# Optimization experiments

Measured on AMD Instinct MI355X. Metric: run time of the kernel, lower is better.

Reference implementation:

```python
import jax, jax.numpy as jnp
import numpy as np

HID = 4096
HEADS = 32
HEAD_DIM = 128
SEQ = 2048
GROUP = 128          # AWQ quantization group size along the input (K) dim
QKV_OUT = 3 * HID
ROPE_BASE = 10000.0


def dequant(qweight, scales, zeros):
    # qweight: [K, N] int; scales/zeros: [K//GROUP, N]
    s = jnp.repeat(scales, GROUP, axis=0)
    z = jnp.repeat(zeros, GROUP, axis=0)
    return (qweight.astype(jnp.float32) - z) * s


def rotate_half(x):
    x1, x2 = jnp.split(x, 2, axis=-1)
    return jnp.concatenate((-x2, x1), axis=-1)


def setup_inputs() -> dict:
    key = jax.random.key(0)
    ks = jax.random.split(key, 8)
    hidden_states = jax.random.normal(ks[0], (1, SEQ, HID), dtype=jnp.float32)
    position_ids = jnp.arange(SEQ, dtype=jnp.int32)[None, :]
    qkv_qweight = jax.random.randint(ks[1], (HID, QKV_OUT), 0, 16, dtype=jnp.int32)
    qkv_scales = jax.random.uniform(ks[2], (HID // GROUP, QKV_OUT), dtype=jnp.float32) * 0.002
    qkv_zeros = jax.random.uniform(ks[3], (HID // GROUP, QKV_OUT), dtype=jnp.float32) * 16.0
    o_qweight = jax.random.randint(ks[4], (HID, HID), 0, 16, dtype=jnp.int32)
    o_scales = jax.random.uniform(ks[5], (HID // GROUP, HID), dtype=jnp.float32) * 0.002
    o_zeros = jax.random.uniform(ks[6], (HID // GROUP, HID), dtype=jnp.float32) * 16.0
    return {"hidden_states": hidden_states, "position_ids": position_ids,
            "qkv_qweight": qkv_qweight, "qkv_scales": qkv_scales, "qkv_zeros": qkv_zeros,
            "o_qweight": o_qweight, "o_scales": o_scales, "o_zeros": o_zeros}


def reference(hidden_states, position_ids, qkv_qweight, qkv_scales, qkv_zeros,
              o_qweight, o_scales, o_zeros):
    b, s, _ = hidden_states.shape
    # --- quantized QKV projection (dequant + GEMM) ---
    w_qkv = dequant(qkv_qweight, qkv_scales, qkv_zeros)        # [HID, 3*HID]
    proj = jnp.einsum('bsk,kn->bsn', hidden_states, w_qkv)     # [b, s, 3*HID]
    xqkv = proj.reshape(b, s, 3, HEADS, HEAD_DIM)
    # [b, h, s, d]
    q = jnp.transpose(xqkv[:, :, 0], (0, 2, 1, 3))
    k = jnp.transpose(xqkv[:, :, 1], (0, 2, 1, 3))
    v = jnp.transpose(xqkv[:, :, 2], (0, 2, 1, 3))
    # --- rotary embedding (no KV cache: kv_seq_len == s) ---
    inv_freq = 1.0 / (ROPE_BASE ** (jnp.arange(0, HEAD_DIM, 2, dtype=jnp.float32) / HEAD_DIM))
    t = jnp.arange(s, dtype=jnp.float32)
    freqs = jnp.outer(t, inv_freq)                             # [s, d/2]
    emb = jnp.concatenate((freqs, freqs), axis=-1)             # [s, d]
    cos = jnp.cos(emb)[position_ids][:, None]                  # [b, 1, s, d]
    sin = jnp.sin(emb)[position_ids][:, None]
    q = q * cos + rotate_half(q) * sin
    k = k * cos + rotate_half(k) * sin
    # --- causal attention (flash_attn_func, padding_mask=None branch) ---
    scale = 1.0 / jnp.sqrt(jnp.float32(HEAD_DIM))
    scores = jnp.einsum('bhqd,bhkd->bhqk', q, k) * scale       # [b, h, s, s]
    causal = jnp.tril(jnp.ones((s, s), dtype=bool))
    scores = jnp.where(causal, scores, jnp.float32(-1e30))
    probs = jax.nn.softmax(scores, axis=-1)
    attn = jnp.einsum('bhqk,bhkd->bhqd', probs, v)             # [b, h, s, d]
    attn = jnp.transpose(attn, (0, 2, 1, 3)).reshape(b, s, HID)
    # --- quantized output projection ---
    w_o = dequant(o_qweight, o_scales, o_zeros)                # [HID, HID]
    out = jnp.einsum('bsk,kn->bsn', attn, w_o)                 # [b, s, HID]
    return out
```

## Files before the change

### kernel.cpp

```cpp
#include <hip/hip_runtime.h>
#include <hip/hip_bf16.h>

#define S_LEN 2048
#define HID_DIM 4096
#define NH 32
#define HD 128
#define NQKV 12288

typedef _Float16 half2v __attribute__((ext_vector_type(2)));
typedef _Float16 half4v __attribute__((ext_vector_type(4)));
typedef _Float16 half8v __attribute__((ext_vector_type(8)));
typedef float f32x4 __attribute__((ext_vector_type(4)));

typedef const __attribute__((address_space(1))) unsigned int* gas_u32;
typedef __attribute__((address_space(3))) unsigned int* las_u32;

__device__ inline void g2lds16(const _Float16* g, _Float16* l) {
  __builtin_amdgcn_global_load_lds((gas_u32)g, (las_u32)l, 16, 0, 0);
}

__device__ inline void store_out(_Float16* p, float v) { *p = (_Float16)v; }
__device__ inline void store_out(float* p, float v) { *p = v; }

__global__ __launch_bounds__(256) void dequant_w(const int* __restrict__ W,
                                                 const float* __restrict__ scal,
                                                 const float* __restrict__ zer,
                                                 _Float16* __restrict__ Wt, int K, int N) {
  __shared__ _Float16 lT[64 * 84];
  const int k0 = blockIdx.y * 64, n0 = blockIdx.x * 64;
  const int tid = threadIdx.x, c = tid & 63, rp = tid >> 6;
  const int g = k0 >> 7;
  const float sc = scal[(size_t)g * N + n0 + c];
  const float zp = zer[(size_t)g * N + n0 + c];
#pragma unroll
  for (int i = 0; i < 8; ++i) {
    const int k = i * 8 + rp * 2;
    const float q0 = (float)W[(size_t)(k0 + k) * N + n0 + c];
    const float q1 = (float)W[(size_t)(k0 + k + 1) * N + n0 + c];
    half2v p;
    p[0] = (_Float16)((q0 - zp) * sc);
    p[1] = (_Float16)((q1 - zp) * sc);
    *(half2v*)&lT[c * 84 + k] = p;
  }
  __syncthreads();
  const int kc = tid & 7, nr0 = tid >> 3;
#pragma unroll
  for (int i = 0; i < 2; ++i) {
    const int n = nr0 + 32 * i;
    union { half8v v8; half4v v4[2]; } u;
    u.v4[0] = *(const half4v*)&lT[n * 84 + kc * 8];
    u.v4[1] = *(const half4v*)&lT[n * 84 + kc * 8 + 4];
    *(half8v*)&Wt[(size_t)(n0 + n) * K + k0 + kc * 8] = u.v8;
  }
}

__global__ __launch_bounds__(256) void conv_a(const float* __restrict__ A, _Float16* __restrict__ Af) {
  const int i = blockIdx.x * 256 + threadIdx.x;
  const float4 t = ((const float4*)A)[i];
  half4v r;
  r[0] = (_Float16)t.x; r[1] = (_Float16)t.y; r[2] = (_Float16)t.z; r[3] = (_Float16)t.w;
  ((half4v*)Af)[i] = r;
}

template <typename CT>
__global__ __launch_bounds__(256) void gemm_f16(const _Float16* __restrict__ A,
                                                const _Float16* __restrict__ Bt,
                                                CT* __restrict__ C, int M, int N, int K) {
  __shared__ _Float16 lA[128 * 32];
  __shared__ _Float16 lB[128 * 32];

  const int tid = threadIdx.x;
  const int wave = tid >> 6, lane = tid & 63;
  const int quad = lane >> 4, l16 = lane & 15;
  const int wr = wave >> 1, wc = wave & 1;
  const int mb = blockIdx.y, nb = blockIdx.x;

  f32x4 acc[4][4];
  const f32x4 zero4 = {0.f, 0.f, 0.f, 0.f};
#pragma unroll
  for (int mt = 0; mt < 4; ++mt)
#pragma unroll
    for (int nt = 0; nt < 4; ++nt) acc[mt][nt] = zero4;

  const _Float16* Ab = A + (size_t)(mb * 128) * K;
  const _Float16* Bb = Bt + (size_t)(nb * 128) * K;
  const int lrow = lane >> 2;
  const int lkc = ((lane & 3) ^ ((lane >> 3) & 3)) * 8;
  const int sq = (quad ^ ((l16 >> 1) & 3)) * 8;

  for (int k0 = 0; k0 < K; k0 += 32) {
#pragma unroll
    for (int p = 0; p < 2; ++p) {
      const int issue = wave * 2 + p;
      const int row = issue * 16 + lrow;
      g2lds16(Ab + (size_t)row * K + k0 + lkc, &lA[issue * 512]);
      g2lds16(Bb + (size_t)row * K + k0 + lkc, &lB[issue * 512]);
    }
    __syncthreads();

    half8v af[4], bf[4];
#pragma unroll
    for (int mt = 0; mt < 4; ++mt) af[mt] = *(half8v*)&lA[(wr * 64 + mt * 16 + l16) * 32 + sq];
#pragma unroll
    for (int nt = 0; nt < 4; ++nt) bf[nt] = *(half8v*)&lB[(wc * 64 + nt * 16 + l16) * 32 + sq];
#pragma unroll
    for (int mt = 0; mt < 4; ++mt)
#pragma unroll
      for (int nt = 0; nt < 4; ++nt)
        acc[mt][nt] = __builtin_amdgcn_mfma_f32_16x16x32_f16(af[mt], bf[nt], acc[mt][nt], 0, 0, 0);
    __syncthreads();
  }

#pragma unroll
  for (int mt = 0; mt < 4; ++mt) {
#pragma unroll
    for (int nt = 0; nt < 4; ++nt) {
#pragma unroll
      for (int i = 0; i < 4; ++i) {
        const int row = mb * 128 + wr * 64 + mt * 16 + quad * 4 + i;
        const int col = nb * 128 + wc * 64 + nt * 16 + l16;
        store_out(C + (size_t)row * N + col, acc[mt][nt][i]);
      }
    }
  }
}

__global__ __launch_bounds__(256) void rope_kernel(const _Float16* __restrict__ proj,
                                                   const int* __restrict__ pos,
                                                   _Float16* __restrict__ Q, _Float16* __restrict__ K,
                                                   _Float16* __restrict__ Vt) {
  const int h = blockIdx.x, sb = blockIdx.y;
  const int tid = threadIdx.x;
  const int s0 = sb * 64;

#pragma unroll
  for (int it = 0; it < 16; ++it) {
    const int idx = it * 256 + tid;
    const int sl = idx >> 6, j = idx & 63;
    const int s = s0 + sl;
    const float p = (float)pos[s];
    const float invrev = exp2f(-0.20762050593045455f * (float)j) * 0.15915494309189535f;
    const float rev = p * invrev;
    const float frac = rev - floorf(rev);
    const float sn = __builtin_amdgcn_sinf(frac);
    const float cs = __builtin_amdgcn_cosf(frac);
    const _Float16* rp = proj + (size_t)s * NQKV + h * HD;
    {
      const float x1 = (float)rp[j], x2 = (float)rp[j + 64];
      _Float16* qp = Q + ((size_t)h * S_LEN + s) * HD;
      qp[j] = (_Float16)(x1 * cs - x2 * sn);
      qp[j + 64] = (_Float16)(x2 * cs + x1 * sn);
    }
    {
      const float x1 = (float)rp[HID_DIM + j], x2 = (float)rp[HID_DIM + j + 64];
      _Float16* kp = K + ((size_t)h * S_LEN + s) * HD;
      kp[j] = (_Float16)(x1 * cs - x2 * sn);
      kp[j + 64] = (_Float16)(x2 * cs + x1 * sn);
    }
  }

  __shared__ _Float16 lV[64 * 132];
#pragma unroll
  for (int r = 0; r < 4; ++r) {
    const int cid = r * 256 + tid;
    const int sl = cid >> 4;
    const int d0 = (cid & 15) * 8;
    const _Float16* vp = proj + (size_t)(s0 + sl) * NQKV + 2 * HID_DIM + h * HD + d0;
    *(half4v*)&lV[sl * 132 + d0] = *(const half4v*)vp;
    *(half4v*)&lV[sl * 132 + d0 + 4] = *(const half4v*)(vp + 4);
  }
  __syncthreads();
#pragma unroll
  for (int it = 0; it < 32; ++it) {
    const int d = it * 4 + (tid >> 6);
    const int sl = tid & 63;
    Vt[((size_t)h * HD + d) * S_LEN + s0 + sl] = lV[sl * 132 + d];
  }
}

__global__ __launch_bounds__(256) void flash_attn(const _Float16* __restrict__ Q,
                                                  const _Float16* __restrict__ Km,
                                                  const _Float16* __restrict__ Vt,
                                                  _Float16* __restrict__ O) {
  __shared__ _Float16 lK[32 * 128];
  __shared__ _Float16 lV[128 * 32];
  __shared__ _Float16 lP[4][2][16 * 40];
  const int h = blockIdx.y;
  const int xb = blockIdx.x;
  const int qb = (xb & 1) ? (15 - (xb >> 1)) : (xb >> 1);
  const int tid = threadIdx.x;
  const int wave = tid >> 6, lane = tid & 63;
  const int quad = lane >> 4, l16 = lane & 15;
  const int q0w = qb * 128 + wave * 32;
  const float scale = 0.08838834764831845f;

  const _Float16* Qh = Q + (size_t)h * S_LEN * HD;
  const _Float16* Kh = Km + (size_t)h * S_LEN * HD;
  const _Float16* Vh = Vt + (size_t)h * HD * S_LEN;

  const int kRow0 = wave * 8 + (lane >> 4);
  const int kSlot = lane & 15;
  const int vRow0 = wave * 32 + (lane >> 2);
  const int vSlot = lane & 3;

  half8v qf[2][4];
#pragma unroll
  for (int r = 0; r < 2; ++r)
#pragma unroll
    for (int c = 0; c < 4; ++c)
      qf[r][c] = *(const half8v*)&Qh[(size_t)(q0w + r * 16 + l16) * HD + c * 32 + quad * 8];

  const f32x4 zero4 = {0.f, 0.f, 0.f, 0.f};
  f32x4 o[2][8];
  f32x4 lp[2];
#pragma unroll
  for (int r = 0; r < 2; ++r) {
    lp[r] = zero4;
#pragma unroll
    for (int c = 0; c < 8; ++c) o[r][c] = zero4;
  }

  const int ntiles = 4 * qb + 4;
  for (int kt = 0; kt < ntiles; ++kt) {
#pragma unroll
    for (int i = 0; i < 2; ++i) {
      const int row = kRow0 + i * 4;
      const int ck = kSlot ^ (row & 15);
      g2lds16(Kh + (size_t)(kt * 32 + row) * HD + ck * 8, &lK[(wave * 8 + i * 4) * 128]);
    }
#pragma unroll
    for (int i = 0; i < 2; ++i) {
      const int row = vRow0 + i * 16;
      const int cv = vSlot ^ ((row >> 1) & 3);
      g2lds16(Vh + (size_t)row * S_LEN + kt * 32 + cv * 8, &lV[(wave * 32 + i * 16) * 32]);
    }
    __syncthreads();

    half8v kf[2][4];
#pragma unroll
    for (int hf = 0; hf < 2; ++hf)
#pragma unroll
      for (int c = 0; c < 4; ++c) {
        const int slot = (c * 4 + quad) ^ l16;
        kf[hf][c] = *(const half8v*)&lK[(hf * 16 + l16) * 128 + slot * 8];
      }
    half8v vf[8];
#pragma unroll
    for (int c = 0; c < 8; ++c) {
      const int slot = quad ^ ((l16 >> 1) & 3);
      vf[c] = *(const half8v*)&lV[(c * 16 + l16) * 32 + slot * 8];
    }

    f32x4 s[2][2];
#pragma unroll
    for (int r = 0; r < 2; ++r)
#pragma unroll
      for (int hf = 0; hf < 2; ++hf) {
        s[r][hf] = zero4;
#pragma unroll
        for (int c = 0; c < 4; ++c)
          s[r][hf] = __builtin_amdgcn_mfma_f32_16x16x32_f16(qf[r][c], kf[hf][c], s[r][hf], 0, 0, 0);
      }

#pragma unroll
    for (int r = 0; r < 2; ++r) {
      float p0[4], p1[4];
#pragma unroll
      for (int i = 0; i < 4; ++i) {
        const int row = q0w + r * 16 + quad * 4 + i;
        const int col0 = kt * 32 + l16, col1 = col0 + 16;
        const float e0 = __expf(s[r][0][i] * scale);
        const float e1 = __expf(s[r][1][i] * scale);
        p0[i] = (col0 <= row) ? e0 : 0.f;
        p1[i] = (col1 <= row) ? e1 : 0.f;
        lp[r][i] += p0[i] + p1[i];
      }
      _Float16* pw = lP[wave][r];
#pragma unroll
      for (int i = 0; i < 4; ++i) {
        pw[(quad * 4 + i) * 40 + l16] = (_Float16)p0[i];
        pw[(quad * 4 + i) * 40 + l16 + 16] = (_Float16)p1[i];
      }
    }
    half8v pa[2];
#pragma unroll
    for (int r = 0; r < 2; ++r) pa[r] = *(half8v*)&lP[wave][r][l16 * 40 + quad * 8];

#pragma unroll
    for (int c = 0; c < 8; ++c)
#pragma unroll
      for (int r = 0; r < 2; ++r)
        o[r][c] = __builtin_amdgcn_mfma_f32_16x16x32_f16(pa[r], vf[c], o[r][c], 0, 0, 0);

    __syncthreads();
  }

#pragma unroll
  for (int r = 0; r < 2; ++r) {
    f32x4 ls = lp[r];
#pragma unroll
    for (int off = 1; off < 16; off <<= 1) {
#pragma unroll
      for (int i = 0; i < 4; ++i) ls[i] += __shfl_xor(ls[i], off);
    }
    f32x4 inv;
#pragma unroll
    for (int i = 0; i < 4; ++i) inv[i] = 1.f / ls[i];
#pragma unroll
    for (int c = 0; c < 8; ++c) {
#pragma unroll
      for (int i = 0; i < 4; ++i) {
        const int row = q0w + r * 16 + quad * 4 + i;
        O[(size_t)row * HID_DIM + h * HD + c * 16 + l16] = (_Float16)(o[r][c][i] * inv[i]);
      }
    }
  }
}

extern "C" void kernel_launch(void* const* d_in, const int* in_sizes, int n_in,
                              void* d_out, int out_size, void* d_ws, size_t ws_size,
                              hipStream_t stream) {
  const float* hidden = (const float*)d_in[0];
  const int* pos = (const int*)d_in[1];
  const int* qkv_w = (const int*)d_in[2];
  const float* qkv_s = (const float*)d_in[3];
  const float* qkv_z = (const float*)d_in[4];
  const int* o_w = (const int*)d_in[5];
  const float* o_s = (const float*)d_in[6];
  const float* o_z = (const float*)d_in[7];

  char* ws = (char*)d_ws;
  _Float16* Wt_qkv = (_Float16*)(ws + 0);
  _Float16* Qb = (_Float16*)(ws + 0);
  _Float16* Kb = (_Float16*)(ws + 16777216);
  _Float16* Vtb = (_Float16*)(ws + 33554432);
  _Float16* Af16 = (_Float16*)(ws + 100663296);
  _Float16* attn = (_Float16*)(ws + 100663296);
  _Float16* proj = (_Float16*)(ws + 117440512);
  _Float16* Wt_o = (_Float16*)(ws + 117440512);
  float* out = (float*)d_out;

  hipLaunchKernelGGL(dequant_w, dim3(192, 64), dim3(256), 0, stream,
                     qkv_w, qkv_s, qkv_z, Wt_qkv, 4096, 12288);
  hipLaunchKernelGGL(conv_a, dim3(8192), dim3(256), 0, stream, hidden, Af16);
  hipLaunchKernelGGL((gemm_f16<_Float16>), dim3(96, 16), dim3(256), 0, stream,
                     Af16, Wt_qkv, proj, 2048, 12288, 4096);
  hipLaunchKernelGGL(rope_kernel, dim3(32, 32), dim3(256), 0, stream, proj, pos, Qb, Kb, Vtb);
  hipLaunchKernelGGL(dequant_w, dim3(64, 64), dim3(256), 0, stream,
                     o_w, o_s, o_z, Wt_o, 4096, 4096);
  hipLaunchKernelGGL(flash_attn, dim3(16, 32), dim3(256), 0, stream, Qb, Kb, Vtb, attn);
  hipLaunchKernelGGL((gemm_f16<float>), dim3(32, 16), dim3(256), 0, stream,
                     attn, Wt_o, out, 2048, 4096, 4096);
}
```

Measured before the change: 854.4 us.

## Rewrite GEMM with 256x128 tiles, multi-buffered LDS prefetch and 8-wave blocks

```diff
diff --git a/kernel.cpp b/kernel.cpp
--- a/kernel.cpp
+++ b/kernel.cpp
@@ -18,9 +18,6 @@
 __device__ inline void g2lds16(const _Float16* g, _Float16* l) {
   __builtin_amdgcn_global_load_lds((gas_u32)g, (las_u32)l, 16, 0, 0);
 }
-
-__device__ inline void store_out(_Float16* p, float v) { *p = (_Float16)v; }
-__device__ inline void store_out(float* p, float v) { *p = v; }
 
 __global__ __launch_bounds__(256) void dequant_w(const int* __restrict__ W,
                                                  const float* __restrict__ scal,
@@ -62,67 +59,128 @@
   ((half4v*)Af)[i] = r;
 }
 
+__device__ inline void stage128x64(const _Float16* __restrict__ gp, int K,
+                                   _Float16* lp, int wave, int stR, int stC) {
+  g2lds16(gp + (size_t)(wave * 16 + stR) * K + stC, lp + (wave * 2) * 512);
+  g2lds16(gp + (size_t)(wave * 16 + 8 + stR) * K + stC, lp + (wave * 2 + 1) * 512);
+}
+
 template <typename CT>
-__global__ __launch_bounds__(256) void gemm_f16(const _Float16* __restrict__ A,
-                                                const _Float16* __restrict__ Bt,
-                                                CT* __restrict__ C, int M, int N, int K) {
-  __shared__ _Float16 lA[128 * 32];
-  __shared__ _Float16 lB[128 * 32];
+__global__ __launch_bounds__(512, 2) void gemm_f16(const _Float16* __restrict__ A,
+                                                   const _Float16* __restrict__ Bt,
+                                                   CT* __restrict__ C, int M, int N, int K) {
+  __shared__ _Float16 sA[3][2][128 * 64];
+  __shared__ _Float16 sB[2][128 * 64];
 
   const int tid = threadIdx.x;
   const int wave = tid >> 6, lane = tid & 63;
   const int quad = lane >> 4, l16 = lane & 15;
-  const int wr = wave >> 1, wc = wave & 1;
-  const int mb = blockIdx.y, nb = blockIdx.x;
-
-  f32x4 acc[4][4];
+  const int wr = wave >> 2;
+  const int wc = wave & 3;
+  const int NT = K >> 6;
+
+  const _Float16* Ab = A + (size_t)(blockIdx.y * 256) * K;
+  const _Float16* Bb = Bt + (size_t)(blockIdx.x * 128) * K;
+
+  const int stR = lane >> 3;
+  const int stC = ((lane & 7) ^ stR) << 3;
+  const int fx = l16 & 7;
+
+#define LDA8(buf, half, r, c) (*(const half8v*)&sA[buf][half][(r) * 64 + (((c) ^ fx) << 3)])
+#define LDB8(buf, r, c) (*(const half8v*)&sB[buf][(r) * 64 + (((c) ^ fx) << 3)])
+
+  f32x4 acc[8][2];
   const f32x4 zero4 = {0.f, 0.f, 0.f, 0.f};
 #pragma unroll
-  for (int mt = 0; mt < 4; ++mt)
-#pragma unroll
-    for (int nt = 0; nt < 4; ++nt) acc[mt][nt] = zero4;
-
-  const _Float16* Ab = A + (size_t)(mb * 128) * K;
-  const _Float16* Bb = Bt + (size_t)(nb * 128) * K;
-  const int lrow = lane >> 2;
-  const int lkc = ((lane & 3) ^ ((lane >> 3) & 3)) * 8;
-  const int sq = (quad ^ ((l16 >> 1) & 3)) * 8;
-
-  for (int k0 = 0; k0 < K; k0 += 32) {
-#pragma unroll
-    for (int p = 0; p < 2; ++p) {
-      const int issue = wave * 2 + p;
-      const int row = issue * 16 + lrow;
-      g2lds16(Ab + (size_t)row * K + k0 + lkc, &lA[issue * 512]);
-      g2lds16(Bb + (size_t)row * K + k0 + lkc, &lB[issue * 512]);
-    }
-    __syncthreads();
-
-    half8v af[4], bf[4];
-#pragma unroll
-    for (int mt = 0; mt < 4; ++mt) af[mt] = *(half8v*)&lA[(wr * 64 + mt * 16 + l16) * 32 + sq];
-#pragma unroll
-    for (int nt = 0; nt < 4; ++nt) bf[nt] = *(half8v*)&lB[(wc * 64 + nt * 16 + l16) * 32 + sq];
-#pragma unroll
-    for (int mt = 0; mt < 4; ++mt)
-#pragma unroll
-      for (int nt = 0; nt < 4; ++nt)
-        acc[mt][nt] = __builtin_amdgcn_mfma_f32_16x16x32_f16(af[mt], bf[nt], acc[mt][nt], 0, 0, 0);
-    __syncthreads();
-  }
-
-#pragma unroll
-  for (int mt = 0; mt < 4; ++mt) {
-#pragma unroll
-    for (int nt = 0; nt < 4; ++nt) {
-#pragma unroll
-      for (int i = 0; i < 4; ++i) {
-        const int row = mb * 128 + wr * 64 + mt * 16 + quad * 4 + i;
-        const int col = nb * 128 + wc * 64 + nt * 16 + l16;
-        store_out(C + (size_t)row * N + col, acc[mt][nt][i]);
-      }
-    }
-  }
+  for (int am = 0; am < 8; ++am)
+#pragma unroll
+    for (int nb = 0; nb < 2; ++nb) acc[am][nb] = zero4;
+
+  stage128x64(Ab, K, &sA[0][0][0], wave, stR, stC);
+  stage128x64(Ab + (size_t)128 * K, K, &sA[0][1][0], wave, stR, stC);
+  stage128x64(Bb, K, &sB[0][0], wave, stR, stC);
+  stage128x64(Ab + 64, K, &sA[1][0][0], wave, stR, stC);
+  stage128x64(Ab + (size_t)128 * K + 64, K, &sA[1][1][0], wave, stR, stC);
+  stage128x64(Bb + 64, K, &sB[1][0], wave, stR, stC);
+  asm volatile("s_waitcnt vmcnt(6)" ::: "memory");
+  __builtin_amdgcn_s_barrier();
+
+  int bA = 0;
+  for (int t = 0; t < NT; ++t) {
+    const int bB = t & 1;
+    const int bA2 = (bA + 2 >= 3) ? bA - 1 : bA + 2;
+
+    half8v af[4][2], bf[2][2];
+#pragma unroll
+    for (int mb = 0; mb < 4; ++mb)
+#pragma unroll
+      for (int ks = 0; ks < 2; ++ks)
+        af[mb][ks] = LDA8(bA, wr, mb * 16 + l16, ks * 4 + quad);
+#pragma unroll
+    for (int nb = 0; nb < 2; ++nb)
+#pragma unroll
+      for (int ks = 0; ks < 2; ++ks)
+        bf[nb][ks] = LDB8(bB, wc * 32 + nb * 16 + l16, ks * 4 + quad);
+    if (t + 2 < NT) {
+      const _Float16* Ap = Ab + (size_t)(t + 2) * 64;
+      stage128x64(Ap, K, &sA[bA2][0][0], wave, stR, stC);
+      stage128x64(Ap + (size_t)128 * K, K, &sA[bA2][1][0], wave, stR, stC);
+    }
+    __builtin_amdgcn_s_barrier();
+    asm volatile("s_waitcnt lgkmcnt(0)" ::: "memory");
+    __builtin_amdgcn_sched_barrier(0);
+    __builtin_amdgcn_s_setprio(1);
+#pragma unroll
+    for (int mb = 0; mb < 4; ++mb)
+#pragma unroll
+      for (int nb = 0; nb < 2; ++nb)
+#pragma unroll
+        for (int ks = 0; ks < 2; ++ks)
+          acc[mb][nb] =
+              __builtin_amdgcn_mfma_f32_16x16x32_f16(af[mb][ks], bf[nb][ks], acc[mb][nb], 0, 0, 0);
+    __builtin_amdgcn_s_setprio(0);
+    __builtin_amdgcn_s_barrier();
+
+#pragma unroll
+    for (int mb = 0; mb < 4; ++mb)
+#pragma unroll
+      for (int ks = 0; ks < 2; ++ks)
+        af[mb][ks] = LDA8(bA, wr, 64 + mb * 16 + l16, ks * 4 + quad);
+    if (t + 2 < NT) {
+      stage128x64(Bb + (size_t)(t + 2) * 64, K, &sB[bB][0], wave, stR, stC);
+      asm volatile("s_waitcnt vmcnt(6)" ::: "memory");
+    } else if (t + 1 < NT) {
+      asm volatile("s_waitcnt vmcnt(0)" ::: "memory");
+    }
+    __builtin_amdgcn_s_barrier();
+    asm volatile("s_waitcnt lgkmcnt(0)" ::: "memory");
+    __builtin_amdgcn_sched_barrier(0);
+    __builtin_amdgcn_s_setprio(1);
+#pragma unroll
+    for (int mb = 0; mb < 4; ++mb)
+#pragma unroll
+      for (int nb = 0; nb < 2; ++nb)
+#pragma unroll
+        for (int ks = 0; ks < 2; ++ks)
+          acc[4 + mb][nb] = __builtin_amdgcn_mfma_f32_16x16x32_f16(af[mb][ks], bf[nb][ks],
+                                                                   acc[4 + mb][nb], 0, 0, 0);
+    __builtin_amdgcn_s_setprio(0);
+    __builtin_amdgcn_s_barrier();
+
+    bA = (bA + 1 >= 3) ? 0 : bA + 1;
+  }
+
+  const int rbase = blockIdx.y * 256 + wr * 128 + quad * 4;
+  const int cbase = blockIdx.x * 128 + wc * 32 + l16;
+#pragma unroll
+  for (int am = 0; am < 8; ++am)
+#pragma unroll
+    for (int nb = 0; nb < 2; ++nb)
+#pragma unroll
+      for (int i = 0; i < 4; ++i)
+        C[(size_t)(rbase + am * 16 + i) * N + cbase + nb * 16] = (CT)acc[am][nb][i];
+#undef LDA8
+#undef LDB8
 }
 
 __global__ __launch_bounds__(256) void rope_kernel(const _Float16* __restrict__ proj,
@@ -343,12 +401,12 @@
   hipLaunchKernelGGL(dequant_w, dim3(192, 64), dim3(256), 0, stream,
                      qkv_w, qkv_s, qkv_z, Wt_qkv, 4096, 12288);
   hipLaunchKernelGGL(conv_a, dim3(8192), dim3(256), 0, stream, hidden, Af16);
-  hipLaunchKernelGGL((gemm_f16<_Float16>), dim3(96, 16), dim3(256), 0, stream,
+  hipLaunchKernelGGL((gemm_f16<_Float16>), dim3(96, 8), dim3(512), 0, stream,
                      Af16, Wt_qkv, proj, 2048, 12288, 4096);
   hipLaunchKernelGGL(rope_kernel, dim3(32, 32), dim3(256), 0, stream, proj, pos, Qb, Kb, Vtb);
   hipLaunchKernelGGL(dequant_w, dim3(64, 64), dim3(256), 0, stream,
                      o_w, o_s, o_z, Wt_o, 4096, 4096);
   hipLaunchKernelGGL(flash_attn, dim3(16, 32), dim3(256), 0, stream, Qb, Kb, Vtb, attn);
-  hipLaunchKernelGGL((gemm_f16<float>), dim3(32, 16), dim3(256), 0, stream,
+  hipLaunchKernelGGL((gemm_f16<float>), dim3(32, 8), dim3(512), 0, stream,
                      attn, Wt_o, out, 2048, 4096, 4096);
 }
```

New measurement: 770.1 us. -9.9%, faster.
